# Kernel tuning notes

Hardware: AMD Instinct MI355X
Metric: run time of the kernel (lower is better)

Reference implementation:

```python
import jax, jax.numpy as jnp
import numpy as np

KS = 3          # kernel_size
NH = 6          # num_heads
NUM_TOK = KS ** 3  # 27 neighbors per query


def setup_inputs() -> dict:
    key = jax.random.key(0)
    k1, k2, k3 = jax.random.split(key, 3)
    q = jax.random.normal(k1, (1, 40, 40, 40, 96), dtype=jnp.float32)
    k = jax.random.normal(k2, (1, 40, 40, 40, 96), dtype=jnp.float32)
    rpb = jax.random.normal(k3, (NH, KS, KS, KS), dtype=jnp.float32) * 0.02
    return {"q": q, "k": k, "rpb": rpb}


def _offsets():
    # torch.arange(-3//2+1, 3//2+1) == arange(-1, 2); meshgrid 'ij'; stacked -> [27, 3]
    r = jnp.arange(-1, 2, dtype=jnp.float32)
    g = jnp.stack(jnp.meshgrid(r, r, r, indexing="ij"), axis=-1)
    return g.reshape(NUM_TOK, 3)


def reference(q, k, rpb):
    B, H, W, T, C = q.shape
    hd = C // NH
    scale = hd ** -0.5
    N = H * W * T

    # queries: [B, N, nh, hd], pre-scaled
    qh = q.reshape(B, N, NH, hd) * scale

    # zero-pad keys by 1 voxel on each spatial side (matches nnf.pad on channels-first k)
    kp = jnp.pad(jnp.transpose(k, (0, 4, 1, 2, 3)),
                 ((0, 0), (0, 0), (1, 1), (1, 1), (1, 1)))

    # 27 shifted views == torch unfold over a 3x3x3 window (i slowest, matches grid order)
    wins = [kp[:, :, i:i + H, j:j + W, l:l + T]
            for i in range(KS) for j in range(KS) for l in range(KS)]
    Kw = jnp.stack(wins, axis=2)                 # [B, C, 27, H, W, T]
    Kw = Kw.reshape(B, NH, hd, NUM_TOK, N)        # [B, nh, hd, 27, N]

    # attention logits over the 27-token neighborhood
    attn = jnp.einsum("bnhd,bhdkn->bnhk", qh, Kw)  # [B, N, nh, 27]
    attn = attn + rpb.reshape(NH, NUM_TOK)[None, None, :, :]  # relative position bias
    attn = jax.nn.softmax(attn, axis=-1)

    # expected displacement: weighted sum of integer offsets -> [B, N, nh, 3]
    x = jnp.einsum("bnhk,kc->bnhc", attn, _offsets())
    x = x.reshape(B, H, W, T, NH * 3)
    return jnp.transpose(x, (0, 4, 1, 2, 3))      # [B, nh*3, H, W, T]
```

## Files before the change

### kernel.cpp

```cpp
#include <hip/hip_runtime.h>

typedef _Float16 hh2 __attribute__((ext_vector_type(2)));

#define DH 40
#define DW 40
#define DT 40
#define NC 96
#define NH 6
#define HD 16
#define NTOK 27
#define NVOX (DH * DW * DT)

#define TX 8
#define TY 4
#define TZ 8
#define HX 10
#define HY 6
#define HZ 10
#define NHALO 600

#define NBLK 750
#define GRID 752
#define PER_XCD 94

__device__ __forceinline__ float dot2acc(hh2 a, hh2 b, float c) {
    return __builtin_amdgcn_fdot2(a, b, c, false);
}
__device__ __forceinline__ unsigned int pkbits(float a, float b) {
    return __builtin_bit_cast(unsigned int, __builtin_amdgcn_cvt_pkrtz(a, b));
}
__device__ __forceinline__ hh2 asz(unsigned int u) {
    return __builtin_bit_cast(hh2, u);
}

union I4H {
    int4 v;
    hh2 h[4];
};

__device__ __forceinline__ int swz(int n, int m) {
    return (4 * n + m) ^ (n & 7);
}

__global__ __launch_bounds__(512, 6) void natt_disp_kernel(
    const float* __restrict__ q,
    const float* __restrict__ k,
    const float* __restrict__ rpb,
    float* __restrict__ out)
{
    __shared__ int4 s_k[NHALO * 4];

    const int job = (blockIdx.x & 7) * PER_XCD + (blockIdx.x >> 3);
    if (job >= NBLK) return;

    const int hp   = job % 3;
    const int tile = job / 3;
    const int tz = tile % 5;
    const int ty = (tile / 5) % 10;
    const int tx = tile / 50;
    const int x0 = tx * TX, y0 = ty * TY, z0 = tz * TZ;

    const int tid = threadIdx.x;
    const int v = tid & 255;
    const int p = tid >> 8;

    const int lz = v & 7;
    const int ly = (v >> 3) & 3;
    const int lx = v >> 5;
    const int vox = ((x0 + lx) * DW + (y0 + ly)) * DT + (z0 + lz);

    const float LOG2E = 1.44269504f;
    const int ps = __builtin_amdgcn_readfirstlane(p);
    const int h = 2 * hp + ps;
    float rk[NTOK];
    {
        const float* rb = rpb + h * NTOK;
        #pragma unroll
        for (int kk = 0; kk < NTOK; ++kk) rk[kk] = rb[kk] * LOG2E;
    }

    #pragma unroll
    for (int it = 0; it < 10; ++it) {
        const int jj = tid + it * 512;
        if (jj < NHALO * 8) {
            const int n = jj >> 3;
            const int c = jj & 7;
            const int hx = n / (HY * HZ);
            const int r  = n - hx * (HY * HZ);
            const int hy = r / HZ;
            const int hz = r - hy * HZ;
            const int gx = x0 - 1 + hx;
            const int gy = y0 - 1 + hy;
            const int gz = z0 - 1 + hz;
            uint2 w; w.x = 0u; w.y = 0u;
            if (((unsigned)gx < DH) & ((unsigned)gy < DW) & ((unsigned)gz < DT)) {
                const float4 a = *(const float4*)(
                    k + ((size_t)((gx * DW + gy) * DT + gz)) * NC
                      + hp * 32 + c * 4);
                w.x = pkbits(a.x, a.y);
                w.y = pkbits(a.z, a.w);
            }
            ((uint2*)s_k)[swz(n, c >> 1) * 2 + (c & 1)] = w;
        }
    }

    hh2 qh[8];
    {
        const float4* qs = (const float4*)(q + (size_t)vox * NC
                                             + hp * 32 + p * HD);
        const float4 a = qs[0], b = qs[1], c = qs[2], d = qs[3];
        qh[0] = asz(pkbits(a.x, a.y)); qh[1] = asz(pkbits(a.z, a.w));
        qh[2] = asz(pkbits(b.x, b.y)); qh[3] = asz(pkbits(b.z, b.w));
        qh[4] = asz(pkbits(c.x, c.y)); qh[5] = asz(pkbits(c.z, c.w));
        qh[6] = asz(pkbits(d.x, d.y)); qh[7] = asz(pkbits(d.z, d.w));
    }

    __syncthreads();

    const float SC2 = 0.36067376f;
    float sum = 0.f, sx = 0.f, sy = 0.f, sz = 0.f;

    #pragma unroll
    for (int i = 0; i < 3; ++i) {
        #pragma unroll
        for (int j = 0; j < 3; ++j) {
            const int base = ((lx + i) * HY + (ly + j)) * HZ + lz;
            #pragma unroll
            for (int ll = 0; ll < 3; ++ll) {
                const int n = base + ll;
                const int ph0 = swz(n, 2 * p);
                I4H u0, u1;
                u0.v = s_k[ph0];
                u1.v = s_k[ph0 ^ 1];
                float d = 0.0f;
                d = dot2acc(qh[0], u0.h[0], d);
                d = dot2acc(qh[1], u0.h[1], d);
                d = dot2acc(qh[2], u0.h[2], d);
                d = dot2acc(qh[3], u0.h[3], d);
                d = dot2acc(qh[4], u1.h[0], d);
                d = dot2acc(qh[5], u1.h[1], d);
                d = dot2acc(qh[6], u1.h[2], d);
                d = dot2acc(qh[7], u1.h[3], d);
                const int kk = (i * 3 + j) * 3 + ll;
                const float t = exp2f(fmaf(d, SC2, rk[kk]));
                sum += t;
                if (i == 0) sx -= t; else if (i == 2) sx += t;
                if (j == 0) sy -= t; else if (j == 2) sy += t;
                if (ll == 0) sz -= t; else if (ll == 2) sz += t;
            }
        }
    }

    const float inv = __builtin_amdgcn_rcpf(sum);

    out[((size_t)(h * 3 + 0)) * NVOX + vox] = sx * inv;
    out[((size_t)(h * 3 + 1)) * NVOX + vox] = sy * inv;
    out[((size_t)(h * 3 + 2)) * NVOX + vox] = sz * inv;
}

extern "C" void kernel_launch(void* const* d_in, const int* in_sizes, int n_in,
                              void* d_out, int out_size, void* d_ws, size_t ws_size,
                              hipStream_t stream) {
    const float* q   = (const float*)d_in[0];
    const float* k   = (const float*)d_in[1];
    const float* rpb = (const float*)d_in[2];
    float* out = (float*)d_out;

    natt_disp_kernel<<<GRID, 512, 0, stream>>>(q, k, rpb, out);
}
```

Baseline: 22.83 us.

## Stage K halo via global_load_lds DMA and overlap second head's load with compute

Switches from 512-thread blocks, where each half handles one head, to 256-thread blocks that process two heads one after the other. Each head's K halo is loaded as raw fp32 straight into LDS with global_load_lds, using a zeroed workspace buffer as the source for padding voxels. A separate pass then converts it to a swizzled fp16 buffer. The second head's DMA is issued before the first head's compute so the load latency overlaps the math. This adds an extra memset launch, more LDS use (raw plus f16 buffers), extra barriers and lower per-block parallelism.

```diff
diff --git a/kernel.cpp b/kernel.cpp
--- a/kernel.cpp
+++ b/kernel.cpp
@@ -6,10 +6,9 @@
 #define DW 40
 #define DT 40
 #define NC 96
-#define NH 6
 #define HD 16
 #define NTOK 27
-#define NVOX (DH * DW * DT)
+#define NVOX 64000
 
 #define TX 8
 #define TY 4
@@ -18,6 +17,8 @@
 #define HY 6
 #define HZ 10
 #define NHALO 600
+#define NCHK (NHALO * 4)
+#define NF16 (NHALO * 2)
 
 #define NBLK 750
 #define GRID 752
@@ -31,6 +32,22 @@
 }
 __device__ __forceinline__ hh2 asz(unsigned int u) {
     return __builtin_bit_cast(hh2, u);
+}
+
+#if defined(__has_builtin)
+#if __has_builtin(__builtin_amdgcn_global_load_lds)
+#define HAVE_DMA 1
+#endif
+#endif
+
+__device__ __forceinline__ void dma16(const float* g, int4* l) {
+#ifdef HAVE_DMA
+    __builtin_amdgcn_global_load_lds(
+        (const __attribute__((address_space(1))) void*)g,
+        (__attribute__((address_space(3))) void*)l, 16, 0, 0);
+#else
+    *l = *(const int4*)g;
+#endif
 }
 
 union I4H {
@@ -38,17 +55,15 @@
     hh2 h[4];
 };
 
-__device__ __forceinline__ int swz(int n, int m) {
-    return (4 * n + m) ^ (n & 7);
-}
-
-__global__ __launch_bounds__(512, 6) void natt_disp_kernel(
+__global__ __launch_bounds__(256, 2) void natt_disp_kernel(
     const float* __restrict__ q,
     const float* __restrict__ k,
     const float* __restrict__ rpb,
-    float* __restrict__ out)
+    float* __restrict__ out,
+    const float* __restrict__ zp)
 {
-    __shared__ int4 s_k[NHALO * 4];
+    __shared__ int4 s_raw[NCHK + 32];
+    __shared__ int4 s_f16[NF16];
 
     const int job = (blockIdx.x & 7) * PER_XCD + (blockIdx.x >> 3);
     if (job >= NBLK) return;
@@ -61,101 +76,138 @@
     const int x0 = tx * TX, y0 = ty * TY, z0 = tz * TZ;
 
     const int tid = threadIdx.x;
-    const int v = tid & 255;
-    const int p = tid >> 8;
-
-    const int lz = v & 7;
-    const int ly = (v >> 3) & 3;
-    const int lx = v >> 5;
+    const int lz = tid & 7;
+    const int ly = (tid >> 3) & 3;
+    const int lx = tid >> 5;
     const int vox = ((x0 + lx) * DW + (y0 + ly)) * DT + (z0 + lz);
 
+    const int h0 = 2 * hp, h1 = 2 * hp + 1;
+
     const float LOG2E = 1.44269504f;
-    const int ps = __builtin_amdgcn_readfirstlane(p);
-    const int h = 2 * hp + ps;
-    float rk[NTOK];
+    float rk0[NTOK], rk1[NTOK];
     {
-        const float* rb = rpb + h * NTOK;
-        #pragma unroll
-        for (int kk = 0; kk < NTOK; ++kk) rk[kk] = rb[kk] * LOG2E;
+        const float* rb = rpb + h0 * NTOK;
+        #pragma unroll
+        for (int kk = 0; kk < NTOK; ++kk) rk0[kk] = rb[kk] * LOG2E;
+        #pragma unroll
+        for (int kk = 0; kk < NTOK; ++kk) rk1[kk] = rb[NTOK + kk] * LOG2E;
     }
 
-    #pragma unroll
-    for (int it = 0; it < 10; ++it) {
-        const int jj = tid + it * 512;
-        if (jj < NHALO * 8) {
-            const int n = jj >> 3;
-            const int c = jj & 7;
-            const int hx = n / (HY * HZ);
-            const int r  = n - hx * (HY * HZ);
-            const int hy = r / HZ;
-            const int hz = r - hy * HZ;
-            const int gx = x0 - 1 + hx;
-            const int gy = y0 - 1 + hy;
-            const int gz = z0 - 1 + hz;
-            uint2 w; w.x = 0u; w.y = 0u;
-            if (((unsigned)gx < DH) & ((unsigned)gy < DW) & ((unsigned)gz < DT)) {
-                const float4 a = *(const float4*)(
-                    k + ((size_t)((gx * DW + gy) * DT + gz)) * NC
-                      + hp * 32 + c * 4);
-                w.x = pkbits(a.x, a.y);
-                w.y = pkbits(a.z, a.w);
-            }
-            ((uint2*)s_k)[swz(n, c >> 1) * 2 + (c & 1)] = w;
-        }
-    }
-
-    hh2 qh[8];
-    {
-        const float4* qs = (const float4*)(q + (size_t)vox * NC
-                                             + hp * 32 + p * HD);
-        const float4 a = qs[0], b = qs[1], c = qs[2], d = qs[3];
-        qh[0] = asz(pkbits(a.x, a.y)); qh[1] = asz(pkbits(a.z, a.w));
-        qh[2] = asz(pkbits(b.x, b.y)); qh[3] = asz(pkbits(b.z, b.w));
-        qh[4] = asz(pkbits(c.x, c.y)); qh[5] = asz(pkbits(c.z, c.w));
-        qh[6] = asz(pkbits(d.x, d.y)); qh[7] = asz(pkbits(d.z, d.w));
-    }
-
-    __syncthreads();
-
-    const float SC2 = 0.36067376f;
-    float sum = 0.f, sx = 0.f, sy = 0.f, sz = 0.f;
-
-    #pragma unroll
-    for (int i = 0; i < 3; ++i) {
-        #pragma unroll
-        for (int j = 0; j < 3; ++j) {
-            const int base = ((lx + i) * HY + (ly + j)) * HZ + lz;
-            #pragma unroll
-            for (int ll = 0; ll < 3; ++ll) {
-                const int n = base + ll;
-                const int ph0 = swz(n, 2 * p);
-                I4H u0, u1;
-                u0.v = s_k[ph0];
-                u1.v = s_k[ph0 ^ 1];
-                float d = 0.0f;
-                d = dot2acc(qh[0], u0.h[0], d);
-                d = dot2acc(qh[1], u0.h[1], d);
-                d = dot2acc(qh[2], u0.h[2], d);
-                d = dot2acc(qh[3], u0.h[3], d);
-                d = dot2acc(qh[4], u1.h[0], d);
-                d = dot2acc(qh[5], u1.h[1], d);
-                d = dot2acc(qh[6], u1.h[2], d);
-                d = dot2acc(qh[7], u1.h[3], d);
-                const int kk = (i * 3 + j) * 3 + ll;
-                const float t = exp2f(fmaf(d, SC2, rk[kk]));
-                sum += t;
-                if (i == 0) sx -= t; else if (i == 2) sx += t;
-                if (j == 0) sy -= t; else if (j == 2) sy += t;
-                if (ll == 0) sz -= t; else if (ll == 2) sz += t;
+    auto dma_stage = [&](const float* kh) {
+        #pragma unroll
+        for (int it = 0; it < 10; ++it) {
+            const int ch = tid + it * 256;
+            if (ch < NCHK) {
+                const int n = ch >> 2;
+                const int c = ch & 3;
+                const int hx = n / (HY * HZ);
+                const int r  = n - hx * (HY * HZ);
+                const int hy = r / HZ;
+                const int hz = r - hy * HZ;
+                const int gx = x0 - 1 + hx;
+                const int gy = y0 - 1 + hy;
+                const int gz = z0 - 1 + hz;
+                const float* src = zp;
+                if (((unsigned)gx < DH) & ((unsigned)gy < DW) & ((unsigned)gz < DT))
+                    src = kh + ((size_t)((gx * DW + gy) * DT + gz)) * NC + c * 4;
+                dma16(src, &s_raw[ch]);
             }
         }
-    }
-
-    const float inv = __builtin_amdgcn_rcpf(sum);
-
-    out[((size_t)(h * 3 + 0)) * NVOX + vox] = sx * inv;
-    out[((size_t)(h * 3 + 1)) * NVOX + vox] = sy * inv;
-    out[((size_t)(h * 3 + 2)) * NVOX + vox] = sz * inv;
+    };
+
+    auto convert = [&]() {
+        #pragma unroll
+        for (int it = 0; it < 5; ++it) {
+            const int f = tid + it * 256;
+            if (f < NF16) {
+                const int n = f >> 1;
+                const int r = n - (n / (HY * HZ)) * (HY * HZ);
+                const int hy = r / HZ;
+                const float4 r0 = *(const float4*)&s_raw[2 * f];
+                const float4 r1 = *(const float4*)&s_raw[2 * f + 1];
+                int4 w;
+                w.x = (int)pkbits(r0.x, r0.y);
+                w.y = (int)pkbits(r0.z, r0.w);
+                w.z = (int)pkbits(r1.x, r1.y);
+                w.w = (int)pkbits(r1.z, r1.w);
+                s_f16[f ^ (hy & 1)] = w;
+            }
+        }
+    };
+
+    const float SC2 = 0.36067376f;
+    auto compute = [&](hh2 (&qh)[8], float (&rk)[NTOK], int hh) {
+        float sum = 0.f, sx = 0.f, sy = 0.f, sz = 0.f;
+        #pragma unroll
+        for (int i = 0; i < 3; ++i) {
+            #pragma unroll
+            for (int j = 0; j < 3; ++j) {
+                const int base = ((lx + i) * HY + (ly + j)) * HZ + lz;
+                const int p = (ly + j) & 1;
+                #pragma unroll
+                for (int ll = 0; ll < 3; ++ll) {
+                    const int n = base + ll;
+                    I4H u0, u1;
+                    u0.v = s_f16[(n * 2 + 0) ^ p];
+                    u1.v = s_f16[(n * 2 + 1) ^ p];
+                    float d = 0.0f;
+                    d = dot2acc(qh[0], u0.h[0], d);
+                    d = dot2acc(qh[1], u0.h[1], d);
+                    d = dot2acc(qh[2], u0.h[2], d);
+                    d = dot2acc(qh[3], u0.h[3], d);
+                    d = dot2acc(qh[4], u1.h[0], d);
+                    d = dot2acc(qh[5], u1.h[1], d);
+                    d = dot2acc(qh[6], u1.h[2], d);
+                    d = dot2acc(qh[7], u1.h[3], d);
+                    const int kk = (i * 3 + j) * 3 + ll;
+                    const float t = exp2f(fmaf(d, SC2, rk[kk]));
+                    sum += t;
+                    if (i == 0) sx -= t; else if (i == 2) sx += t;
+                    if (j == 0) sy -= t; else if (j == 2) sy += t;
+                    if (ll == 0) sz -= t; else if (ll == 2) sz += t;
+                }
+            }
+        }
+        const float inv = __builtin_amdgcn_rcpf(sum);
+        out[((size_t)(hh * 3 + 0)) * NVOX + vox] = sx * inv;
+        out[((size_t)(hh * 3 + 1)) * NVOX + vox] = sy * inv;
+        out[((size_t)(hh * 3 + 2)) * NVOX + vox] = sz * inv;
+    };
+
+    const float4* q0p = (const float4*)(q + (size_t)vox * NC + h0 * HD);
+    const float4 a0 = q0p[0], b0 = q0p[1], c0 = q0p[2], d0 = q0p[3];
+
+    dma_stage(k + h0 * HD);
+
+    hh2 qhA[8];
+    qhA[0] = asz(pkbits(a0.x, a0.y)); qhA[1] = asz(pkbits(a0.z, a0.w));
+    qhA[2] = asz(pkbits(b0.x, b0.y)); qhA[3] = asz(pkbits(b0.z, b0.w));
+    qhA[4] = asz(pkbits(c0.x, c0.y)); qhA[5] = asz(pkbits(c0.z, c0.w));
+    qhA[6] = asz(pkbits(d0.x, d0.y)); qhA[7] = asz(pkbits(d0.z, d0.w));
+
+    __syncthreads();
+    convert();
+    __syncthreads();
+
+    const float4* q1p = (const float4*)(q + (size_t)vox * NC + h1 * HD);
+    const float4 a1 = q1p[0], b1 = q1p[1], c1 = q1p[2], d1 = q1p[3];
+
+    dma_stage(k + h1 * HD);
+    __builtin_amdgcn_sched_barrier(0);
+
+    hh2 qhB[8];
+    qhB[0] = asz(pkbits(a1.x, a1.y)); qhB[1] = asz(pkbits(a1.z, a1.w));
+    qhB[2] = asz(pkbits(b1.x, b1.y)); qhB[3] = asz(pkbits(b1.z, b1.w));
+    qhB[4] = asz(pkbits(c1.x, c1.y)); qhB[5] = asz(pkbits(c1.z, c1.w));
+    qhB[6] = asz(pkbits(d1.x, d1.y)); qhB[7] = asz(pkbits(d1.z, d1.w));
+
+    compute(qhA, rk0, h0);
+
+    __syncthreads();
+    convert();
+    __syncthreads();
+
+    compute(qhB, rk1, h1);
 }
 
 extern "C" void kernel_launch(void* const* d_in, const int* in_sizes, int n_in,
@@ -166,5 +218,7 @@
     const float* rpb = (const float*)d_in[2];
     float* out = (float*)d_out;
 
-    natt_disp_kernel<<<GRID, 512, 0, stream>>>(q, k, rpb, out);
-}
+    hipMemsetAsync(d_ws, 0, 256, stream);
+    natt_disp_kernel<<<GRID, 256, 0, stream>>>(q, k, rpb, out,
+                                               (const float*)d_ws);
+}
```

New measurement: 40.37 us. +76.9%, slower.
